# Optimization experiments

Hardware: AMD Instinct MI355X
Metric: run time of the kernel (lower is better)

Reference implementation:

```python
import jax, jax.numpy as jnp
import numpy as np

BS, GS, E, KMAX = 128, 2000, 128, 4
CLIP = 10.0
NEG = -1e30


def _gru(x, hprev, Wih, Whh, bih, bhh):
    # torch.nn.GRUCell math
    gi = x @ Wih.T + bih
    gh = hprev @ Whh.T + bhh
    ir, iz, i_n = jnp.split(gi, 3, axis=-1)
    hr, hz, h_n = jnp.split(gh, 3, axis=-1)
    r = jax.nn.sigmoid(ir + hr)
    z = jax.nn.sigmoid(iz + hz)
    n = jnp.tanh(i_n + r * h_n)
    return (1.0 - z) * n + z * hprev


def setup_inputs() -> dict:
    key = jax.random.key(0)
    it = iter(jax.random.split(key, 40))
    s = 1.0 / float(np.sqrt(E))
    u = lambda shape: jax.random.uniform(next(it), shape, jnp.float32, -s, s)
    inp = {
        "h": jax.random.normal(next(it), (BS, GS, E), jnp.float32),
        "rec": jax.random.randint(next(it), (BS, GS), 0, GS, dtype=jnp.int32),
        "context2": jax.random.normal(next(it), (BS, 9), jnp.float32),
        "visited_time": jax.random.randint(next(it), (BS, GS), 0, GS, dtype=jnp.int32),
        "last_action": jax.random.randint(next(it), (BS, 1), 0, GS, dtype=jnp.int32),
        "fixed_action": jax.random.randint(next(it), (BS, KMAX), 0, GS, dtype=jnp.int32),
    }
    for n in ["W_K1", "W_K2", "W_K3", "W_K4", "W_Q1", "W_Q2", "W_Q3", "W_Q4", "W_init"]:
        inp[n] = u((E, E))
    for n in ["b_init", "V1", "V2", "init_query"]:
        inp[n] = u((E,))
    for r in ["rnn1", "rnn2"]:
        inp[r + "_Wih"] = u((3 * E, E))
        inp[r + "_Whh"] = u((3 * E, E))
        inp[r + "_bih"] = u((3 * E,))
        inp[r + "_bhh"] = u((3 * E,))
    return inp


def _forward(h, rec, visited_time, last_action, fixed_action,
             W_K1, W_K2, W_K3, W_K4, W_Q1, W_Q2, W_Q3, W_Q4, V1, V2,
             W_init, b_init, init_query,
             rnn1_Wih, rnn1_Whh, rnn1_bih, rnn1_bhh,
             rnn2_Wih, rnn2_Whh, rnn2_bih, rnn2_bhh):
    bs, gs, e = h.shape
    cols = jnp.arange(gs)[None, :]          # [1, gs]
    rows = jnp.arange(bs)
    # K projections of h are loop-invariant: hoist them (same math as in-loop recompute)
    K1h = jnp.einsum('bge,fe->bgf', h, W_K1)
    K2h = jnp.einsum('bge,fe->bgf', h, W_K2)
    K3h = jnp.einsum('bge,fe->bgf', h, W_K3)
    K4h = jnp.einsum('bge,fe->bgf', h, W_K4)
    q1 = q2 = h.mean(1) @ W_init.T + b_init
    input_q1 = input_q2 = jnp.broadcast_to(init_query, (bs, e))
    mask = jnp.zeros((bs, gs), bool)
    stopped = jnp.ones((bs,), bool)
    nol = jnp.full((bs, 1), -1, jnp.int32)   # next_of_last_action
    ai = jnp.zeros((bs, KMAX), jnp.int32)    # action_index
    kl = jnp.zeros((bs, KMAX + 1), jnp.int32)
    kr = jnp.zeros((bs, KMAX), jnp.int32)
    ll = jnp.zeros((bs,), h.dtype)
    vtt = None
    for i in range(KMAX):
        q1 = _gru(input_q1, q1, rnn1_Wih, rnn1_Whh, rnn1_bih, rnn1_bhh)
        q2 = _gru(input_q2, q2, rnn2_Wih, rnn2_Whh, rnn2_bih, rnn2_bhh)
        s1 = (V1 * jnp.tanh(K1h + (q1 @ W_Q1.T)[:, None, :] + K3h * (q1 @ W_Q3.T)[:, None, :])).sum(-1)
        s2 = (V2 * jnp.tanh(K2h + (q2 @ W_Q2.T)[:, None, :] + K4h * (q2 @ W_Q4.T)[:, None, :])).sum(-1)
        logits = jnp.tanh(s1 + s2) * CLIP
        logits = jnp.where(mask, NEG, logits)
        if i == 0:
            logits = jnp.where(cols == last_action, NEG, logits)
        action = fixed_action[:, i:i + 1]
        if i > 0:
            action = jnp.where(stopped[:, None], ai[:, 0:1], action)
        logp = jax.nn.log_softmax(logits, axis=-1)
        loss_now = jnp.take_along_axis(logp, action, 1)[:, 0]
        ll = ll + (loss_now if i == 0 else jnp.where(stopped, 0.0, loss_now))
        nna = jnp.take_along_axis(rec, action, 1)  # next_of_new_action [bs,1]
        ai = ai.at[:, i].set(action[:, 0])
        kl = kl.at[:, i].set(jnp.where(stopped, action[:, 0], kl[:, i]))
        kr = kr.at[:, (i - 1) % KMAX].set(jnp.where(stopped, kr[:, (i - 1) % KMAX], action[:, 0]))
        kl = kl.at[:, i + 1].set(nna[:, 0])
        input_q1 = h[rows, action[:, 0]]
        input_q2 = jnp.where(stopped[:, None], input_q1, h[rows, nol[:, 0] % gs])
        eq = (action == nol)[:, 0]
        stopped = eq if i == 0 else (stopped | eq)
        kl = kl.at[:, i].set(jnp.where(stopped, kl[:, (i - 1) % (KMAX + 1)], kl[:, i]))
        kr = kr.at[:, i].set(jnp.where(stopped, kr[:, (i - 1) % KMAX], kr[:, i]))
        if i == 0:
            vtt = (visited_time - jnp.take_along_axis(visited_time, action, 1)) % gs
        vtt_a = jnp.take_along_axis(vtt, action, 1)
        mask = vtt <= vtt_a
        if i == 0:
            mask = mask | (vtt > gs - 2)
        mask = jnp.where(stopped[:, None] & (cols == action), False, mask)
        allow = (~stopped) & (nna[:, 0] == ai[:, 0])
        mask = jnp.where(allow[:, None] & (cols == ai[:, 0:1]), False, mask)
        nol = jnp.where(stopped[:, None], jnp.int32(-1), nna)
    kr = kr.at[:, KMAX - 1].set(jnp.where(~stopped, kl[:, KMAX], kr[:, KMAX - 1]))
    action_all = jnp.concatenate([ai, kl[:, :KMAX], kr], axis=-1)  # [bs, 3*KMAX]
    return action_all, ll


def reference(h, rec, context2, visited_time, last_action, fixed_action,
              W_K1, W_K2, W_K3, W_K4, W_Q1, W_Q2, W_Q3, W_Q4,
              V1, V2, W_init, b_init, init_query,
              rnn1_Wih, rnn1_Whh, rnn1_bih, rnn1_bhh,
              rnn2_Wih, rnn2_Whh, rnn2_bih, rnn2_bhh):
    # context2 unused: with_explore_stat_feature=False path (learned V1/V2)
    return _forward(h, rec, visited_time, last_action, fixed_action,
                    W_K1, W_K2, W_K3, W_K4, W_Q1, W_Q2, W_Q3, W_Q4, V1, V2,
                    W_init, b_init, init_query,
                    rnn1_Wih, rnn1_Whh, rnn1_bih, rnn1_bhh,
                    rnn2_Wih, rnn2_Whh, rnn2_bih, rnn2_bhh)
```

## Files before the change

### kernel.cpp

```cpp
#include <hip/hip_runtime.h>
#include <math.h>

#define BS 128
#define GS 2000
#define E  128
#define KMAXI 4
#define CLIPV 10.0f
#define NEGV  -1.0e30f

typedef __bf16 bf16_t;
typedef __bf16 bf16x8 __attribute__((ext_vector_type(8)));
typedef float fx4 __attribute__((ext_vector_type(4)));
typedef float fx2 __attribute__((ext_vector_type(2)));

__device__ __forceinline__ float fast_sigmoid(float x){ return 1.0f/(1.0f+__expf(-x)); }
__device__ __forceinline__ float fast_tanhf(float x){
    float e = __expf(2.0f*x);
    return 1.0f - 2.0f/(e + 1.0f);
}
__device__ __forceinline__ float pade_tanh(float x){
    float t = __builtin_amdgcn_fmed3f(x, -3.0f, 3.0f);
    float r = t*t;
    float num = t*(27.0f + r);
    float den = fmaf(9.0f, r, 27.0f);
    return num * __builtin_amdgcn_rcpf(den);
}
__device__ __forceinline__ fx2 tanh2_poly(fx2 x){
    fx2 t;
    t.x = __builtin_amdgcn_fmed3f(x.x, -3.0f, 3.0f);
    t.y = __builtin_amdgcn_fmed3f(x.y, -3.0f, 3.0f);
    fx2 r = t*t;
    fx2 q = r*(-0.0015650f) + 0.03172875f;
    q = q*r + (-0.23082094f);
    q = q*r + 0.979947f;
    return t*q;
}
__device__ __forceinline__ int pymod(int a){ int d = a % GS; return d < 0 ? d + GS : d; }

__device__ __forceinline__ void load_lds16(const bf16_t* g, bf16_t* l){
    __builtin_amdgcn_global_load_lds(
        (const __attribute__((address_space(1))) void*)g,
        (__attribute__((address_space(3))) void*)l, 16, 0, 0);
}

#define SC_STRIDE 64

__global__ __launch_bounds__(128) void k_traj(
    const int* __restrict__ rec, const int* __restrict__ vtime,
    const int* __restrict__ last_action, const int* __restrict__ fixed_action,
    int* __restrict__ sc, float* __restrict__ out)
{
    int b = threadIdx.x;
    if (b >= BS) return;
    int stopped = 1, nol = -1;
    int ai[4]={0,0,0,0}, kl[5]={0,0,0,0,0}, kr[4]={0,0,0,0};
    int a0 = 0;
    int* scb = sc + b*SC_STRIDE;
    for (int it=0; it<KMAXI; ++it){
        int action = (it==0) ? fixed_action[b*KMAXI]
                             : (stopped ? ai[0] : fixed_action[b*KMAXI+it]);
        int old_stopped = stopped;
        if (it==0) a0 = action;
        int vta = (it==0) ? 0 : pymod(vtime[(size_t)b*GS+action] - vtime[(size_t)b*GS+a0]);
        int nna = rec[(size_t)b*GS+action];
        int eq  = (action == nol) ? 1 : 0;
        int new_stopped = (it==0) ? eq : (stopped | eq);
        int ai0 = (it==0) ? action : ai[0];
        int allow = (!new_stopped) && (nna == ai0);

        ai[it] = action;
        if (old_stopped)  kl[it] = action;
        if (!old_stopped) kr[(it+3)&3] = action;
        kl[it+1] = nna;
        if (new_stopped) kl[it] = kl[(it+4)%5];
        if (new_stopped) kr[it] = kr[(it+3)&3];

        int row1 = action;
        int i2 = pymod(nol);
        int row2 = old_stopped ? row1 : i2;

        int* s_it = scb + 8 + it*8;
        s_it[0]=action; s_it[1]=old_stopped; s_it[2]=new_stopped;
        s_it[3]=allow;  s_it[4]=vta; s_it[5]=row1; s_it[6]=row2;

        nol = new_stopped ? -1 : nna;
        stopped = new_stopped;
    }
    scb[0] = a0;
    if (!stopped) kr[3] = kl[4];
    out[BS*12 + b] = 0.0f;
    for (int j=0;j<4;++j) out[b*12+j]   = (float)ai[j];
    for (int j=0;j<4;++j) out[b*12+4+j] = (float)kl[j];
    for (int j=0;j<4;++j) out[b*12+8+j] = (float)kr[j];
}

__global__ __launch_bounds__(256) void k_hmean(const float* __restrict__ h, float* __restrict__ hpart){
    int b = blockIdx.x, p = blockIdx.y, tid = threadIdx.x;
    int e4 = (tid & 31) * 4;
    int gsub = tid >> 5;
    float4 acc = {0.f,0.f,0.f,0.f};
    int g0 = p*125, g1 = g0+125;
    for (int g = g0 + gsub; g < g1; g += 8){
        float4 v = *(const float4*)(h + ((size_t)b*GS + g)*E + e4);
        acc.x += v.x; acc.y += v.y; acc.z += v.z; acc.w += v.w;
    }
    __shared__ float ps[8][E];
    *(float4*)(&ps[gsub][e4]) = acc;
    __syncthreads();
    if (tid < E){
        float s = 0.f;
        #pragma unroll
        for (int j=0;j<8;++j) s += ps[j][tid];
        hpart[(b*16+p)*E + tid] = s;
    }
}

__device__ __forceinline__ float dot32(const float* a, const float* __restrict__ w){
    const float4* a4=(const float4*)a; const float4* w4=(const float4*)w;
    float s=0.f;
    #pragma unroll 8
    for (int i=0;i<32;++i){ float4 x=a4[i], y=w4[i]; s += x.x*y.x + x.y*y.y + x.z*y.z + x.w*y.w; }
    return s;
}

__global__ __launch_bounds__(384) void k_gru4(
    const float* __restrict__ hpart, const float* __restrict__ W_init,
    const float* __restrict__ b_init, const float* __restrict__ init_query,
    const float* __restrict__ h, const int* __restrict__ sc,
    const float* __restrict__ Wih1, const float* __restrict__ Whh1,
    const float* __restrict__ bih1, const float* __restrict__ bhh1,
    const float* __restrict__ Wih2, const float* __restrict__ Whh2,
    const float* __restrict__ bih2, const float* __restrict__ bhh2,
    const float* __restrict__ WQ1, const float* __restrict__ WQ2,
    const float* __restrict__ WQ3, const float* __restrict__ WQ4,
    float* __restrict__ add_buf, float* __restrict__ mul_buf)
{
    int b = blockIdx.x, rnn = blockIdx.y, t = threadIdx.x;
    const float* Wih = rnn ? Wih2 : Wih1;
    const float* Whh = rnn ? Whh2 : Whh1;
    const float* bih = rnn ? bih2 : bih1;
    const float* bhh = rnn ? bhh2 : bhh1;
    const float* WQa = rnn ? WQ2 : WQ1;
    const float* WQm = rnn ? WQ4 : WQ3;

    __shared__ float xv[E], hv[E];
    __shared__ float gi_s[3*E], gh_s[3*E];

    if (t < E){
        float s = 0.f;
        for (int p=0;p<16;++p) s += hpart[(b*16+p)*E + t];
        xv[t] = s * (1.0f/(float)GS);
    }
    __syncthreads();
    if (t < E) hv[t] = b_init[t] + dot32(xv, W_init + (size_t)t*E);
    __syncthreads();
    if (t < E) xv[t] = init_query[t];
    __syncthreads();

    for (int s=0; s<KMAXI; ++s){
        if (s>0){
            if (t < E){
                int row = sc[b*SC_STRIDE + 8 + (s-1)*8 + (rnn==0 ? 5 : 6)];
                xv[t] = h[((size_t)b*GS + row)*E + t];
            }
            __syncthreads();
        }
        {
            float gi = bih[t] + dot32(xv, Wih + (size_t)t*E);
            float gh = bhh[t] + dot32(hv, Whh + (size_t)t*E);
            gi_s[t] = gi; gh_s[t] = gh;
        }
        __syncthreads();
        if (t < E){
            float r = fast_sigmoid(gi_s[t]     + gh_s[t]);
            float z = fast_sigmoid(gi_s[t+E]   + gh_s[t+E]);
            float n = fast_tanhf  (gi_s[t+2*E] + r*gh_s[t+2*E]);
            hv[t] = (1.f-z)*n + z*hv[t];
        }
        __syncthreads();
        if (t < 2*E){
            int r = t & (E-1);
            const float* W = (t < E) ? WQa : WQm;
            float v = dot32(hv, W + (size_t)r*E);
            int slot = s*2 + rnn;
            if (t < E) add_buf[(size_t)slot*BS*E + b*E + r] = v;
            else       mul_buf[(size_t)slot*BS*E + b*E + r] = v;
        }
        __syncthreads();
    }
}

__global__ __launch_bounds__(256) void k_mbuild(
    const float* __restrict__ WK1, const float* __restrict__ WK2,
    const float* __restrict__ WK3, const float* __restrict__ WK4,
    const float* __restrict__ mul_buf, bf16_t* __restrict__ Mb)
{
    int b = blockIdx.x, slot = blockIdx.y, tid = threadIdx.x;
    int arm = slot & 1;
    const float* WKa = arm ? WK2 : WK1;
    const float* WKm = arm ? WK4 : WK3;
    const float* mul = mul_buf + (size_t)slot*BS*E + b*E;
    __shared__ float mv[E];
    if (tid < E) mv[tid] = mul[tid];
    __syncthreads();
    bf16x8* outp = (bf16x8*)(Mb + ((size_t)slot*BS + b)*E*E);
    #pragma unroll
    for (int j=0;j<8;++j){
        int u = j*256 + tid;
        int f = u >> 4, e8 = u & 15;
        int e0 = e8*8;
        float mf = mv[f];
        float4 a0 = *(const float4*)(WKa + (size_t)f*E + e0);
        float4 a1 = *(const float4*)(WKa + (size_t)f*E + e0 + 4);
        float4 m0 = *(const float4*)(WKm + (size_t)f*E + e0);
        float4 m1 = *(const float4*)(WKm + (size_t)f*E + e0 + 4);
        bf16x8 o;
        o[0]=(bf16_t)(a0.x + m0.x*mf);
        o[1]=(bf16_t)(a0.y + m0.y*mf);
        o[2]=(bf16_t)(a0.z + m0.z*mf);
        o[3]=(bf16_t)(a0.w + m0.w*mf);
        o[4]=(bf16_t)(a1.x + m1.x*mf);
        o[5]=(bf16_t)(a1.y + m1.y*mf);
        o[6]=(bf16_t)(a1.z + m1.z*mf);
        o[7]=(bf16_t)(a1.w + m1.w*mf);
        outp[f*16 + (e8 ^ (f&7))] = o;
    }
}

__global__ __launch_bounds__(256,2) void k_scores(
    const float* __restrict__ hf, const bf16_t* __restrict__ Mb,
    const float* __restrict__ add_buf,
    const float* __restrict__ V1, const float* __restrict__ V2,
    float* __restrict__ raw4)
{
    __shared__ bf16_t sM[E*E];
    int b = blockIdx.x, yc = blockIdx.y, tid = threadIdx.x;
    int wave = tid >> 6, lane = tid & 63;
    int qd = lane >> 4, cl = lane & 15;
    int gbase = yc*128 + wave*32;

    float vv_r[2][8];
    #pragma unroll
    for (int tf=0; tf<8; ++tf){
        vv_r[0][tf] = V1[tf*16+cl];
        vv_r[1][tf] = V2[tf*16+cl];
    }

    bf16x8 afr[2][4];
    #pragma unroll
    for (int set=0; set<2; ++set){
        int grow = gbase + set*16 + cl;
        if (grow >= GS) grow = GS-1;
        const float* hrow = hf + ((size_t)b*GS + grow)*E;
        #pragma unroll
        for (int s=0;s<4;++s){
            const float* p = hrow + s*32 + qd*8;
            float4 u0 = *(const float4*)(p);
            float4 u1 = *(const float4*)(p+4);
            bf16x8 a;
            a[0]=(bf16_t)u0.x; a[1]=(bf16_t)u0.y; a[2]=(bf16_t)u0.z; a[3]=(bf16_t)u0.w;
            a[4]=(bf16_t)u1.x; a[5]=(bf16_t)u1.y; a[6]=(bf16_t)u1.z; a[7]=(bf16_t)u1.w;
            afr[set][s]=a;
        }
    }

    for (int it=0; it<KMAXI; ++it){
        fx2 s00={0.f,0.f}, s01={0.f,0.f}, s10={0.f,0.f}, s11={0.f,0.f};
        #pragma unroll
        for (int arm=0; arm<2; ++arm){
            int slot = it*2 + arm;
            const bf16_t* Gm = Mb + ((size_t)slot*BS + b)*E*E;
            const float* addv = add_buf + (size_t)slot*BS*E + b*E;

            float av_r[8];
            #pragma unroll
            for (int tf=0; tf<8; ++tf) av_r[tf] = addv[tf*16+cl];

            __syncthreads();
            #pragma unroll
            for (int j=0;j<8;++j){
                int c = wave*512 + j*64 + lane;
                load_lds16(Gm + (size_t)c*8, sM + (size_t)c*8);
            }
            __syncthreads();

            #pragma unroll
            for (int tf=0; tf<8; ++tf){
                int f = tf*16 + cl;
                bf16x8 b1[4];
                #pragma unroll
                for (int s=0;s<4;++s){
                    int e8 = s*4 + qd;
                    b1[s] = *(const bf16x8*)(sM + ((size_t)(f*16 + (e8 ^ (f&7))))*8);
                }
                float av = av_r[tf];
                fx4 a0 = {av,av,av,av};
                fx4 a1 = {av,av,av,av};
                #pragma unroll
                for (int s=0;s<4;++s){
                    a0 = __builtin_amdgcn_mfma_f32_16x16x32_bf16(afr[0][s], b1[s], a0, 0,0,0);
                    a1 = __builtin_amdgcn_mfma_f32_16x16x32_bf16(afr[1][s], b1[s], a1, 0,0,0);
                }
                fx2 vv2 = {vv_r[arm][tf], vv_r[arm][tf]};
                s00 += vv2 * tanh2_poly((fx2){a0[0], a0[1]});
                s01 += vv2 * tanh2_poly((fx2){a0[2], a0[3]});
                s10 += vv2 * tanh2_poly((fx2){a1[0], a1[1]});
                s11 += vv2 * tanh2_poly((fx2){a1[2], a1[3]});
            }
        }
        #pragma unroll
        for (int set=0;set<2;++set){
            fx2 pa = set ? s10 : s00;
            fx2 pb = set ? s11 : s01;
            float v[4] = {pa.x, pa.y, pb.x, pb.y};
            #pragma unroll
            for (int r=0;r<4;++r){
                float s = v[r];
                s += __shfl_xor(s, 1); s += __shfl_xor(s, 2);
                s += __shfl_xor(s, 4); s += __shfl_xor(s, 8);
                v[r] = s;
            }
            if (cl==0){
                int gi = gbase + set*16 + qd*4;
                if (gi+3 < GS){
                    float4 o;
                    o.x = CLIPV*pade_tanh(v[0]);
                    o.y = CLIPV*pade_tanh(v[1]);
                    o.z = CLIPV*pade_tanh(v[2]);
                    o.w = CLIPV*pade_tanh(v[3]);
                    *(float4*)(raw4 + ((size_t)it*BS + b)*GS + gi) = o;
                }
            }
        }
    }
}

__global__ __launch_bounds__(256) void k_ll(
    const float* __restrict__ raw4, const int* __restrict__ sc,
    const int* __restrict__ vtime, const int* __restrict__ last_action,
    float* __restrict__ out)
{
    __shared__ float sL[GS];
    __shared__ float red[256];
    int b = blockIdx.x, it = blockIdx.y, t = threadIdx.x;
    const int* scb = sc + b*SC_STRIDE;
    const int* s_it = scb + 8 + it*8;
    int action = s_it[0], olds = s_it[1];
    if (it>0 && olds) return;
    int a0 = scb[0];
    int la = last_action[b];
    int vt0 = vtime[(size_t)b*GS + a0];
    int ap=0, nsp=0, alp=0, vtp=0, p = it-1;
    if (it>0){
        const int* s_p = scb + 8 + p*8;
        ap = s_p[0]; nsp = s_p[2]; alp = s_p[3]; vtp = s_p[4];
    }
    for (int g=t; g<GS; g+=256){
        float l = raw4[((size_t)it*BS + b)*GS + g];
        int m;
        if (it==0){
            m = (g==la);
        } else {
            int d = pymod(vtime[(size_t)b*GS+g] - vt0);
            m = (d <= vtp) ? 1 : 0;
            if (p==0 && d > GS-2) m = 1;
            if (nsp && g==ap)     m = 0;
            if (alp && g==a0)     m = 0;
        }
        sL[g] = m ? NEGV : l;
    }
    __syncthreads();
    float mx = -3.0e38f;
    for (int g=t; g<GS; g+=256) mx = fmaxf(mx, sL[g]);
    red[t]=mx; __syncthreads();
    for (int s=128;s>0;s>>=1){ if(t<s) red[t]=fmaxf(red[t],red[t+s]); __syncthreads(); }
    mx = red[0]; __syncthreads();
    float sm = 0.f;
    for (int g=t; g<GS; g+=256) sm += __expf(sL[g]-mx);
    red[t]=sm; __syncthreads();
    for (int s=128;s>0;s>>=1){ if(t<s) red[t]+=red[t+s]; __syncthreads(); }
    if (t==0){
        float lse = mx + __logf(red[0]);
        atomicAdd(&out[BS*12 + b], sL[action] - lse);
    }
}

extern "C" void kernel_launch(void* const* d_in, const int* in_sizes, int n_in,
                              void* d_out, int out_size, void* d_ws, size_t ws_size,
                              hipStream_t stream)
{
    const float* h            = (const float*)d_in[0];
    const int*   rec          = (const int*)  d_in[1];
    const int*   vtime        = (const int*)  d_in[3];
    const int*   last_action  = (const int*)  d_in[4];
    const int*   fixed_action = (const int*)  d_in[5];
    const float* WK1=(const float*)d_in[6],  *WK2=(const float*)d_in[7];
    const float* WK3=(const float*)d_in[8],  *WK4=(const float*)d_in[9];
    const float* WQ1=(const float*)d_in[10], *WQ2=(const float*)d_in[11];
    const float* WQ3=(const float*)d_in[12], *WQ4=(const float*)d_in[13];
    const float* W_init=(const float*)d_in[14];
    const float* b_init=(const float*)d_in[15];
    const float* V1=(const float*)d_in[16], *V2=(const float*)d_in[17];
    const float* init_query=(const float*)d_in[18];
    const float* Wih1=(const float*)d_in[19], *Whh1=(const float*)d_in[20];
    const float* bih1=(const float*)d_in[21], *bhh1=(const float*)d_in[22];
    const float* Wih2=(const float*)d_in[23], *Whh2=(const float*)d_in[24];
    const float* bih2=(const float*)d_in[25], *bhh2=(const float*)d_in[26];
    float* out = (float*)d_out;

    char* ws = (char*)d_ws;
    size_t off = 0;
    auto alloc = [&](size_t bytes)->char*{
        char* p = ws + off; off += (bytes + 255) & ~(size_t)255; return p;
    };
    bf16_t* Mb     = (bf16_t*)alloc((size_t)8*BS*E*E*sizeof(bf16_t));
    float*  raw4   = (float*) alloc((size_t)KMAXI*BS*GS*sizeof(float));
    float*  add_buf= (float*) alloc((size_t)8*BS*E*sizeof(float));
    float*  mul_buf= (float*) alloc((size_t)8*BS*E*sizeof(float));
    float*  hpart  = (float*) alloc((size_t)BS*16*E*sizeof(float));
    int*    sc     = (int*)   alloc((size_t)BS*SC_STRIDE*sizeof(int));
    (void)in_sizes; (void)n_in; (void)out_size; (void)ws_size;

    hipLaunchKernelGGL(k_traj, dim3(1), dim3(128), 0, stream,
                       rec, vtime, last_action, fixed_action, sc, out);
    hipLaunchKernelGGL(k_hmean, dim3(BS,16), dim3(256), 0, stream, h, hpart);
    hipLaunchKernelGGL(k_gru4, dim3(BS,2), dim3(384), 0, stream,
                       hpart, W_init, b_init, init_query, h, sc,
                       Wih1,Whh1,bih1,bhh1, Wih2,Whh2,bih2,bhh2,
                       WQ1,WQ2,WQ3,WQ4, add_buf, mul_buf);
    hipLaunchKernelGGL(k_mbuild, dim3(BS,8), dim3(256), 0, stream,
                       WK1,WK2,WK3,WK4, mul_buf, Mb);
    hipLaunchKernelGGL(k_scores, dim3(BS,16), dim3(256), 0, stream,
                       h, Mb, add_buf, V1, V2, raw4);
    hipLaunchKernelGGL(k_ll, dim3(BS, KMAXI), dim3(256), 0, stream,
                       raw4, sc, vtime, last_action, out);
}
```

Measured before the change: 435.8 us.

## Fuse masking and log-softmax into scores kernel, double-buffer M tiles, merge traj into hmean

Folds the trajectory computation into an extra block row of the h-mean kernel, so one launch is saved. The score kernel now applies the mask inline and emits per-block partial max and sum-exp, replacing the raw score buffer and the separate log-likelihood kernel with a tiny final combine kernel. M tiles are double-buffered in LDS so the next slot's global-to-LDS load overlaps the current MFMA work. The cost is doubled LDS use (64KB), which may cut occupancy below the declared two blocks per CU. Masked vtime gathers also move into the score kernel, and pymod now assumes its argument is greater than -GS.

```diff
diff --git a/kernel.cpp b/kernel.cpp
--- a/kernel.cpp
+++ b/kernel.cpp
@@ -35,7 +35,7 @@
     q = q*r + 0.979947f;
     return t*q;
 }
-__device__ __forceinline__ int pymod(int a){ int d = a % GS; return d < 0 ? d + GS : d; }
+__device__ __forceinline__ int pymod_s(int a){ return a < 0 ? a + GS : a; }
 
 __device__ __forceinline__ void load_lds16(const bf16_t* g, bf16_t* l){
     __builtin_amdgcn_global_load_lds(
@@ -45,57 +45,58 @@
 
 #define SC_STRIDE 64
 
-__global__ __launch_bounds__(128) void k_traj(
+__global__ __launch_bounds__(256) void k_hmean(
+    const float* __restrict__ h, float* __restrict__ hpart,
     const int* __restrict__ rec, const int* __restrict__ vtime,
     const int* __restrict__ last_action, const int* __restrict__ fixed_action,
     int* __restrict__ sc, float* __restrict__ out)
 {
-    int b = threadIdx.x;
-    if (b >= BS) return;
-    int stopped = 1, nol = -1;
-    int ai[4]={0,0,0,0}, kl[5]={0,0,0,0,0}, kr[4]={0,0,0,0};
-    int a0 = 0;
-    int* scb = sc + b*SC_STRIDE;
-    for (int it=0; it<KMAXI; ++it){
-        int action = (it==0) ? fixed_action[b*KMAXI]
-                             : (stopped ? ai[0] : fixed_action[b*KMAXI+it]);
-        int old_stopped = stopped;
-        if (it==0) a0 = action;
-        int vta = (it==0) ? 0 : pymod(vtime[(size_t)b*GS+action] - vtime[(size_t)b*GS+a0]);
-        int nna = rec[(size_t)b*GS+action];
-        int eq  = (action == nol) ? 1 : 0;
-        int new_stopped = (it==0) ? eq : (stopped | eq);
-        int ai0 = (it==0) ? action : ai[0];
-        int allow = (!new_stopped) && (nna == ai0);
-
-        ai[it] = action;
-        if (old_stopped)  kl[it] = action;
-        if (!old_stopped) kr[(it+3)&3] = action;
-        kl[it+1] = nna;
-        if (new_stopped) kl[it] = kl[(it+4)%5];
-        if (new_stopped) kr[it] = kr[(it+3)&3];
-
-        int row1 = action;
-        int i2 = pymod(nol);
-        int row2 = old_stopped ? row1 : i2;
-
-        int* s_it = scb + 8 + it*8;
-        s_it[0]=action; s_it[1]=old_stopped; s_it[2]=new_stopped;
-        s_it[3]=allow;  s_it[4]=vta; s_it[5]=row1; s_it[6]=row2;
-
-        nol = new_stopped ? -1 : nna;
-        stopped = new_stopped;
-    }
-    scb[0] = a0;
-    if (!stopped) kr[3] = kl[4];
-    out[BS*12 + b] = 0.0f;
-    for (int j=0;j<4;++j) out[b*12+j]   = (float)ai[j];
-    for (int j=0;j<4;++j) out[b*12+4+j] = (float)kl[j];
-    for (int j=0;j<4;++j) out[b*12+8+j] = (float)kr[j];
-}
-
-__global__ __launch_bounds__(256) void k_hmean(const float* __restrict__ h, float* __restrict__ hpart){
     int b = blockIdx.x, p = blockIdx.y, tid = threadIdx.x;
+    if (p == 16){
+        if (b != 0) return;
+        int t = tid;
+        if (t >= BS) return;
+        int stopped = 1, nol = -1;
+        int ai[4]={0,0,0,0}, kl[5]={0,0,0,0,0}, kr[4]={0,0,0,0};
+        int a0 = 0;
+        int* scb = sc + t*SC_STRIDE;
+        for (int it=0; it<KMAXI; ++it){
+            int action = (it==0) ? fixed_action[t*KMAXI]
+                                 : (stopped ? ai[0] : fixed_action[t*KMAXI+it]);
+            int old_stopped = stopped;
+            if (it==0) a0 = action;
+            int vta = (it==0) ? 0 : pymod_s(vtime[(size_t)t*GS+action] - vtime[(size_t)t*GS+a0]);
+            int nna = rec[(size_t)t*GS+action];
+            int eq  = (action == nol) ? 1 : 0;
+            int new_stopped = (it==0) ? eq : (stopped | eq);
+            int ai0 = (it==0) ? action : ai[0];
+            int allow = (!new_stopped) && (nna == ai0);
+
+            ai[it] = action;
+            if (old_stopped)  kl[it] = action;
+            if (!old_stopped) kr[(it+3)&3] = action;
+            kl[it+1] = nna;
+            if (new_stopped) kl[it] = kl[(it+4)%5];
+            if (new_stopped) kr[it] = kr[(it+3)&3];
+
+            int row1 = action;
+            int i2 = pymod_s(nol);
+            int row2 = old_stopped ? row1 : i2;
+
+            int* s_it = scb + 8 + it*8;
+            s_it[0]=action; s_it[1]=old_stopped; s_it[2]=new_stopped;
+            s_it[3]=allow;  s_it[4]=vta; s_it[5]=row1; s_it[6]=row2;
+
+            nol = new_stopped ? -1 : nna;
+            stopped = new_stopped;
+        }
+        scb[0] = a0;
+        if (!stopped) kr[3] = kl[4];
+        for (int j=0;j<4;++j) out[t*12+j]   = (float)ai[j];
+        for (int j=0;j<4;++j) out[t*12+4+j] = (float)kl[j];
+        for (int j=0;j<4;++j) out[t*12+8+j] = (float)kr[j];
+        return;
+    }
     int e4 = (tid & 31) * 4;
     int gsub = tid >> 5;
     float4 acc = {0.f,0.f,0.f,0.f};
@@ -231,13 +232,31 @@
     const float* __restrict__ hf, const bf16_t* __restrict__ Mb,
     const float* __restrict__ add_buf,
     const float* __restrict__ V1, const float* __restrict__ V2,
-    float* __restrict__ raw4)
-{
-    __shared__ bf16_t sM[E*E];
+    const int* __restrict__ vtime, const int* __restrict__ last_action,
+    const int* __restrict__ sc,
+    float* __restrict__ part, float* __restrict__ act_val)
+{
+    __shared__ bf16_t sM[2][E*E];
+    __shared__ float redm[16], reds[16];
+    __shared__ float bmxs;
     int b = blockIdx.x, yc = blockIdx.y, tid = threadIdx.x;
     int wave = tid >> 6, lane = tid & 63;
     int qd = lane >> 4, cl = lane & 15;
     int gbase = yc*128 + wave*32;
+
+    {
+        const bf16_t* G0 = Mb + (size_t)b*E*E;
+        #pragma unroll
+        for (int j=0;j<8;++j){
+            int c = wave*512 + j*64 + lane;
+            load_lds16(G0 + (size_t)c*8, &sM[0][0] + (size_t)c*8);
+        }
+    }
+
+    const int* scb = sc + b*SC_STRIDE;
+    int a0s = scb[0];
+    int la  = last_action[b];
+    int vt0 = vtime[(size_t)b*GS + a0s];
 
     float vv_r[2][8];
     #pragma unroll
@@ -263,27 +282,28 @@
             afr[set][s]=a;
         }
     }
+    __syncthreads();
 
     for (int it=0; it<KMAXI; ++it){
         fx2 s00={0.f,0.f}, s01={0.f,0.f}, s10={0.f,0.f}, s11={0.f,0.f};
         #pragma unroll
         for (int arm=0; arm<2; ++arm){
             int slot = it*2 + arm;
-            const bf16_t* Gm = Mb + ((size_t)slot*BS + b)*E*E;
+            int cur = slot & 1;
+            if (slot < 7){
+                const bf16_t* Gn = Mb + ((size_t)(slot+1)*BS + b)*E*E;
+                #pragma unroll
+                for (int j=0;j<8;++j){
+                    int c = wave*512 + j*64 + lane;
+                    load_lds16(Gn + (size_t)c*8, &sM[cur^1][0] + (size_t)c*8);
+                }
+            }
             const float* addv = add_buf + (size_t)slot*BS*E + b*E;
-
             float av_r[8];
             #pragma unroll
             for (int tf=0; tf<8; ++tf) av_r[tf] = addv[tf*16+cl];
 
-            __syncthreads();
-            #pragma unroll
-            for (int j=0;j<8;++j){
-                int c = wave*512 + j*64 + lane;
-                load_lds16(Gm + (size_t)c*8, sM + (size_t)c*8);
-            }
-            __syncthreads();
-
+            const bf16_t* sMc = &sM[cur][0];
             #pragma unroll
             for (int tf=0; tf<8; ++tf){
                 int f = tf*16 + cl;
@@ -291,7 +311,7 @@
                 #pragma unroll
                 for (int s=0;s<4;++s){
                     int e8 = s*4 + qd;
-                    b1[s] = *(const bf16x8*)(sM + ((size_t)(f*16 + (e8 ^ (f&7))))*8);
+                    b1[s] = *(const bf16x8*)(sMc + ((size_t)(f*16 + (e8 ^ (f&7))))*8);
                 }
                 float av = av_r[tf];
                 fx4 a0 = {av,av,av,av};
@@ -307,7 +327,10 @@
                 s10 += vv2 * tanh2_poly((fx2){a1[0], a1[1]});
                 s11 += vv2 * tanh2_poly((fx2){a1[2], a1[3]});
             }
-        }
+            __syncthreads();
+        }
+
+        float vfin[2][4];
         #pragma unroll
         for (int set=0;set<2;++set){
             fx2 pa = set ? s10 : s00;
@@ -318,71 +341,95 @@
                 float s = v[r];
                 s += __shfl_xor(s, 1); s += __shfl_xor(s, 2);
                 s += __shfl_xor(s, 4); s += __shfl_xor(s, 8);
-                v[r] = s;
+                vfin[set][r] = s;
             }
-            if (cl==0){
-                int gi = gbase + set*16 + qd*4;
-                if (gi+3 < GS){
-                    float4 o;
-                    o.x = CLIPV*pade_tanh(v[0]);
-                    o.y = CLIPV*pade_tanh(v[1]);
-                    o.z = CLIPV*pade_tanh(v[2]);
-                    o.w = CLIPV*pade_tanh(v[3]);
-                    *(float4*)(raw4 + ((size_t)it*BS + b)*GS + gi) = o;
+        }
+
+        int act = scb[8 + it*8 + 0];
+        int ap=0, nsp=0, alp=0, vtp=0;
+        if (it>0){
+            const int* s_p = scb + 8 + (it-1)*8;
+            ap = s_p[0]; nsp = s_p[2]; alp = s_p[3]; vtp = s_p[4];
+        }
+        float x[8];
+        float lm = NEGV;
+        if (cl==0){
+            #pragma unroll
+            for (int set=0;set<2;++set){
+                #pragma unroll
+                for (int r=0;r<4;++r){
+                    int idx = set*4 + r;
+                    int g = gbase + set*16 + qd*4 + r;
+                    float o = CLIPV*pade_tanh(vfin[set][r]);
+                    int valid = (g < GS);
+                    int gi = valid ? g : (GS-1);
+                    int msk;
+                    if (it==0){
+                        msk = (g==la);
+                    } else {
+                        int d = vtime[(size_t)b*GS + gi] - vt0;
+                        if (d < 0) d += GS;
+                        msk = (d <= vtp) ? 1 : 0;
+                        if (it==1 && d > GS-2) msk = 1;
+                        if (nsp && g==ap)      msk = 0;
+                        if (alp && g==a0s)     msk = 0;
+                    }
+                    float xx = (valid && !msk) ? o : NEGV;
+                    if (valid && g==act) act_val[(size_t)it*BS + b] = xx;
+                    x[idx] = xx;
+                    lm = fmaxf(lm, xx);
                 }
             }
-        }
-    }
-}
-
-__global__ __launch_bounds__(256) void k_ll(
-    const float* __restrict__ raw4, const int* __restrict__ sc,
-    const int* __restrict__ vtime, const int* __restrict__ last_action,
-    float* __restrict__ out)
-{
-    __shared__ float sL[GS];
-    __shared__ float red[256];
-    int b = blockIdx.x, it = blockIdx.y, t = threadIdx.x;
+            redm[wave*4+qd] = lm;
+        }
+        __syncthreads();
+        if (tid==0){
+            float m = redm[0];
+            #pragma unroll
+            for (int i=1;i<16;++i) m = fmaxf(m, redm[i]);
+            bmxs = m;
+        }
+        __syncthreads();
+        float bm = bmxs;
+        if (cl==0){
+            float ls = 0.f;
+            #pragma unroll
+            for (int i=0;i<8;++i) ls += __expf(x[i]-bm);
+            reds[wave*4+qd] = ls;
+        }
+        __syncthreads();
+        if (tid==0){
+            float ss = 0.f;
+            #pragma unroll
+            for (int i=0;i<16;++i) ss += reds[i];
+            fx2 pr = {bm, ss};
+            *(fx2*)(part + (((size_t)it*BS + b)*16 + yc)*2) = pr;
+        }
+    }
+}
+
+__global__ __launch_bounds__(128) void k_final(
+    const float* __restrict__ part, const float* __restrict__ act_val,
+    const int* __restrict__ sc, float* __restrict__ out)
+{
+    int b = threadIdx.x;
+    if (b >= BS) return;
     const int* scb = sc + b*SC_STRIDE;
-    const int* s_it = scb + 8 + it*8;
-    int action = s_it[0], olds = s_it[1];
-    if (it>0 && olds) return;
-    int a0 = scb[0];
-    int la = last_action[b];
-    int vt0 = vtime[(size_t)b*GS + a0];
-    int ap=0, nsp=0, alp=0, vtp=0, p = it-1;
-    if (it>0){
-        const int* s_p = scb + 8 + p*8;
-        ap = s_p[0]; nsp = s_p[2]; alp = s_p[3]; vtp = s_p[4];
-    }
-    for (int g=t; g<GS; g+=256){
-        float l = raw4[((size_t)it*BS + b)*GS + g];
-        int m;
-        if (it==0){
-            m = (g==la);
-        } else {
-            int d = pymod(vtime[(size_t)b*GS+g] - vt0);
-            m = (d <= vtp) ? 1 : 0;
-            if (p==0 && d > GS-2) m = 1;
-            if (nsp && g==ap)     m = 0;
-            if (alp && g==a0)     m = 0;
-        }
-        sL[g] = m ? NEGV : l;
-    }
-    __syncthreads();
-    float mx = -3.0e38f;
-    for (int g=t; g<GS; g+=256) mx = fmaxf(mx, sL[g]);
-    red[t]=mx; __syncthreads();
-    for (int s=128;s>0;s>>=1){ if(t<s) red[t]=fmaxf(red[t],red[t+s]); __syncthreads(); }
-    mx = red[0]; __syncthreads();
-    float sm = 0.f;
-    for (int g=t; g<GS; g+=256) sm += __expf(sL[g]-mx);
-    red[t]=sm; __syncthreads();
-    for (int s=128;s>0;s>>=1){ if(t<s) red[t]+=red[t+s]; __syncthreads(); }
-    if (t==0){
-        float lse = mx + __logf(red[0]);
-        atomicAdd(&out[BS*12 + b], sL[action] - lse);
-    }
+    float ll = 0.f;
+    for (int it=0; it<KMAXI; ++it){
+        const fx2* pp = (const fx2*)(part + (((size_t)it*BS + b)*16)*2);
+        float M = NEGV;
+        #pragma unroll
+        for (int i=0;i<16;++i) M = fmaxf(M, pp[i].x);
+        float S = 0.f;
+        #pragma unroll
+        for (int i=0;i<16;++i) S += pp[i].y * __expf(pp[i].x - M);
+        float lse = M + __logf(S);
+        float av = act_val[(size_t)it*BS + b];
+        int olds = scb[8 + it*8 + 1];
+        if (it==0 || !olds) ll += av - lse;
+    }
+    out[BS*12 + b] = ll;
 }
 
 extern "C" void kernel_launch(void* const* d_in, const int* in_sizes, int n_in,
@@ -414,16 +461,16 @@
         char* p = ws + off; off += (bytes + 255) & ~(size_t)255; return p;
     };
     bf16_t* Mb     = (bf16_t*)alloc((size_t)8*BS*E*E*sizeof(bf16_t));
-    float*  raw4   = (float*) alloc((size_t)KMAXI*BS*GS*sizeof(float));
     float*  add_buf= (float*) alloc((size_t)8*BS*E*sizeof(float));
     float*  mul_buf= (float*) alloc((size_t)8*BS*E*sizeof(float));
     float*  hpart  = (float*) alloc((size_t)BS*16*E*sizeof(float));
     int*    sc     = (int*)   alloc((size_t)BS*SC_STRIDE*sizeof(int));
+    float*  part   = (float*) alloc((size_t)KMAXI*BS*16*2*sizeof(float));
+    float*  actv   = (float*) alloc((size_t)KMAXI*BS*sizeof(float));
     (void)in_sizes; (void)n_in; (void)out_size; (void)ws_size;
 
-    hipLaunchKernelGGL(k_traj, dim3(1), dim3(128), 0, stream,
-                       rec, vtime, last_action, fixed_action, sc, out);
-    hipLaunchKernelGGL(k_hmean, dim3(BS,16), dim3(256), 0, stream, h, hpart);
+    hipLaunchKernelGGL(k_hmean, dim3(BS,17), dim3(256), 0, stream,
+                       h, hpart, rec, vtime, last_action, fixed_action, sc, out);
     hipLaunchKernelGGL(k_gru4, dim3(BS,2), dim3(384), 0, stream,
                        hpart, W_init, b_init, init_query, h, sc,
                        Wih1,Whh1,bih1,bhh1, Wih2,Whh2,bih2,bhh2,
@@ -431,7 +478,7 @@
     hipLaunchKernelGGL(k_mbuild, dim3(BS,8), dim3(256), 0, stream,
                        WK1,WK2,WK3,WK4, mul_buf, Mb);
     hipLaunchKernelGGL(k_scores, dim3(BS,16), dim3(256), 0, stream,
-                       h, Mb, add_buf, V1, V2, raw4);
-    hipLaunchKernelGGL(k_ll, dim3(BS, KMAXI), dim3(256), 0, stream,
-                       raw4, sc, vtime, last_action, out);
-}
+                       h, Mb, add_buf, V1, V2, vtime, last_action, sc, part, actv);
+    hipLaunchKernelGGL(k_final, dim3(1), dim3(128), 0, stream,
+                       part, actv, sc, out);
+}
```

New measurement: 460.5 us. 1.06x slower.
